# Performance work log

Hardware: AMD Instinct MI355X
Metric: run time of the kernel (lower is better)

The kernel has to match this reference:

```python
import jax, jax.numpy as jnp
import numpy as np

ALPHA = 0.2  # LeakyReLU negative slope


def setup_inputs() -> dict:
    key = jax.random.key(0)
    k1, k2, k3 = jax.random.split(key, 3)
    N, F_IN, F_OUT = 8192, 128, 64
    inputs = jax.random.normal(k1, (N, F_IN), dtype=jnp.float32)
    # xavier_uniform with gain=1.414
    limW = 1.414 * np.sqrt(6.0 / (F_IN + F_OUT))
    W = jax.random.uniform(k2, (F_IN, F_OUT), minval=-limW, maxval=limW, dtype=jnp.float32)
    lima = 1.414 * np.sqrt(6.0 / (2 * F_OUT + 1))
    a = jax.random.uniform(k3, (2 * F_OUT, 1), minval=-lima, maxval=lima, dtype=jnp.float32)
    return {"inputs": inputs, "W": W, "a": a}


def reference(inputs, W, a):
    F_OUT = W.shape[1]
    h = inputs @ W  # [N, F_out]
    # The torch code concatenates [h_i, h_j] and dots with a; equivalently
    # split a into a1 (for h_i) and a2 (for h_j): e_ij = LeakyReLU(h_i.a1 + h_j.a2)
    a1 = a[:F_OUT, 0]  # [F_out]
    a2 = a[F_OUT:, 0]  # [F_out]
    f1 = h @ a1  # [N]
    f2 = h @ a2  # [N]
    e = jax.nn.leaky_relu(f1[:, None] + f2[None, :], negative_slope=ALPHA)  # [N, N]
    attention = jax.nn.softmax(e, axis=1)  # dense GAT: softmax over all nodes
    # dropout=0.0 / eval mode -> identity
    feature = attention @ h  # [N, F_out]
    return jax.nn.elu(feature)  # concat=True branch
```

## Files before the change

kernel.cpp:

```cpp
#include <hip/hip_runtime.h>

#define NR    8192
#define ALPHA 0.2f
#define NCH   512
#define CSZ   16

__device__ inline unsigned enc_f32(float f) {
    unsigned u = __float_as_uint(f);
    return (u & 0x80000000u) ? ~u : (u | 0x80000000u);
}
__device__ inline float dec_f32(unsigned u) {
    return __uint_as_float((u & 0x80000000u) ? (u ^ 0x80000000u) : ~u);
}

__global__ __launch_bounds__(256) void kA(
    const float* __restrict__ X, const float* __restrict__ W, const float* __restrict__ aa,
    float* __restrict__ H, float* __restrict__ HT, float* __restrict__ F1,
    unsigned* __restrict__ ENC)
{
    __shared__ __align__(16) float xs[16 * 128];
    __shared__ float part[16 * 4 * 64];
    __shared__ float htl[64 * 17];
    const int tid = threadIdx.x, w = tid >> 6, c = tid & 63;
    const int R0 = blockIdx.x * 16;

    float Wreg[32];
#pragma unroll
    for (int e = 0; e < 32; ++e) Wreg[e] = W[(w * 32 + e) * 64 + c];
    {
        const float4* X4 = (const float4*)(X + R0 * 128);
        float4* xs4 = (float4*)xs;
        xs4[tid] = X4[tid];
        xs4[256 + tid] = X4[256 + tid];
    }
    __syncthreads();

    for (int r = 0; r < 16; ++r) {
        const float4* xr4 = (const float4*)&xs[r * 128 + w * 32];
        float acc = 0.f;
#pragma unroll
        for (int e = 0; e < 8; ++e) {
            float4 xv = xr4[e];
            acc = fmaf(xv.x, Wreg[e * 4 + 0], acc);
            acc = fmaf(xv.y, Wreg[e * 4 + 1], acc);
            acc = fmaf(xv.z, Wreg[e * 4 + 2], acc);
            acc = fmaf(xv.w, Wreg[e * 4 + 3], acc);
        }
        part[(r * 4 + w) * 64 + c] = acc;
    }
    __syncthreads();

    const float a1 = aa[c], a2 = aa[64 + c];
    for (int rr = 0; rr < 4; ++rr) {
        const int r = w * 4 + rr, i = R0 + r;
        float h = part[(r * 4 + 0) * 64 + c] + part[(r * 4 + 1) * 64 + c]
                + part[(r * 4 + 2) * 64 + c] + part[(r * 4 + 3) * 64 + c];
        H[i * 64 + c] = h;
        htl[c * 17 + r] = h;
        float v1 = h * a1, v2 = h * a2;
#pragma unroll
        for (int m = 32; m >= 1; m >>= 1) {
            v1 += __shfl_xor(v1, m, 64);
            v2 += __shfl_xor(v2, m, 64);
        }
        if (c == 0) { F1[i] = v1; ENC[i] = enc_f32(v2); }
    }
    __syncthreads();
    {
        const int ct = tid >> 2, rq = tid & 3;
        float4 v = make_float4(htl[ct * 17 + rq * 4 + 0], htl[ct * 17 + rq * 4 + 1],
                               htl[ct * 17 + rq * 4 + 2], htl[ct * 17 + rq * 4 + 3]);
        *(float4*)&HT[ct * NR + R0 + rq * 4] = v;
    }
}

__global__ __launch_bounds__(256) void kB(
    const unsigned* __restrict__ ENC, float* __restrict__ SF2, int* __restrict__ PERM)
{
    __shared__ unsigned cw[4 * 8];
    const int tid = threadIdx.x, bid = blockIdx.x;
    const uint4* E4 = (const uint4*)ENC;

    unsigned long long k64[32];
    {
        const unsigned base = tid * 4;
#pragma unroll
        for (int q = 0; q < 8; ++q) {
            uint4 v = E4[q * 256 + tid];
            const unsigned ib = q * 1024 + base;
            k64[q * 4 + 0] = ((unsigned long long)v.x << 13) | (ib + 0);
            k64[q * 4 + 1] = ((unsigned long long)v.y << 13) | (ib + 1);
            k64[q * 4 + 2] = ((unsigned long long)v.z << 13) | (ib + 2);
            k64[q * 4 + 3] = ((unsigned long long)v.w << 13) | (ib + 3);
        }
    }

    unsigned cnt[8];
#pragma unroll
    for (int jj = 0; jj < 8; ++jj) {
        const int j = bid * 8 + jj;
        const unsigned long long th = ((unsigned long long)ENC[j] << 13) | (unsigned)j;
        unsigned cjj = 0;
#pragma unroll
        for (int q = 0; q < 32; ++q) cjj += (unsigned)(k64[q] < th);
        cnt[jj] = cjj;
    }
#pragma unroll
    for (int jj = 0; jj < 8; ++jj) {
        unsigned v = cnt[jj];
#pragma unroll
        for (int m = 32; m >= 1; m >>= 1) v += (unsigned)__shfl_xor((int)v, m, 64);
        cnt[jj] = v;
    }
    const int w = tid >> 6;
    if ((tid & 63) == 0) {
#pragma unroll
        for (int jj = 0; jj < 8; ++jj) cw[w * 8 + jj] = cnt[jj];
    }
    __syncthreads();
    if (tid < 8) {
        const unsigned r = cw[tid] + cw[8 + tid] + cw[16 + tid] + cw[24 + tid];
        const int j = bid * 8 + tid;
        SF2[r] = dec_f32(ENC[j]);
        PERM[r] = j;
    }
}

__global__ __launch_bounds__(1024) void kC34(
    const float* __restrict__ HT, const float* __restrict__ SF2, const int* __restrict__ PERM,
    float4* __restrict__ SPQJ, float* __restrict__ CHPx, float* __restrict__ CHQx,
    float* __restrict__ cs)
{
    __shared__ float preP[1024], preQ[1024];
    __shared__ float scP[NCH], scQ[NCH];
    const int t = threadIdx.x, cb = blockIdx.x;
    const float fm = SF2[NR - 1];
    float accP = 0.f, accQ = 0.f;

    const float4* S4 = (const float4*)(SF2 + t * 8);
    const int4*   P4 = (const int4*)(PERM + t * 8);
    float4 f0 = S4[0], f1v = S4[1];
    int4   j0 = P4[0], j1 = P4[1];
    float sv[8] = { f0.x, f0.y, f0.z, f0.w, f1v.x, f1v.y, f1v.z, f1v.w };
    int   jx[8] = { j0.x, j0.y, j0.z, j0.w, j1.x, j1.y, j1.z, j1.w };

    if (cb < 64) {
        const float* __restrict__ hcol = HT + cb * NR;
#pragma unroll
        for (int e = 0; e < 8; ++e) {
            const float d = sv[e] - fm;
            const float P = __expf(d), Q = __expf(ALPHA * d);
            const float hv = hcol[jx[e]];
            accP = fmaf(P, hv, accP);
            accQ = fmaf(Q, hv, accQ);
        }
    } else {
#pragma unroll
        for (int e = 0; e < 8; ++e) {
            const float d = sv[e] - fm;
            const float P = __expf(d), Q = __expf(ALPHA * d);
            SPQJ[t * 8 + e] = make_float4(sv[e], P, Q, __int_as_float(jx[e]));
            accP += P; accQ += Q;
        }
        if (t < NCH) cs[t] = SF2[t * CSZ];
    }

    preP[t] = accP; preQ[t] = accQ;
    __syncthreads();
    if (t < NCH) {
        scP[t] = preP[2 * t] + preP[2 * t + 1];
        scQ[t] = preQ[2 * t] + preQ[2 * t + 1];
    }
    __syncthreads();
    for (int off = 1; off < NCH; off <<= 1) {
        float uP = 0.f, uQ = 0.f;
        if (t < NCH && t >= off) { uP = scP[t - off]; uQ = scQ[t - off]; }
        __syncthreads();
        if (t < NCH) { scP[t] += uP; scQ[t] += uQ; }
        __syncthreads();
    }
    if (t < NCH) {
        const float eP = (t > 0) ? scP[t - 1] : 0.f;
        const float eQ = (t > 0) ? scQ[t - 1] : 0.f;
        CHPx[t * 65 + cb] = eP;
        CHQx[t * 65 + cb] = eQ;
        if (t == NCH - 1) { CHPx[NCH * 65 + cb] = scP[t]; CHQx[NCH * 65 + cb] = scQ[t]; }
    }
}

__global__ __launch_bounds__(256) void kD(
    const float* __restrict__ H, const float* __restrict__ F1, const float* __restrict__ SF2,
    const float4* __restrict__ SPQJ, const float* __restrict__ CHPx,
    const float* __restrict__ CHQx, const float* __restrict__ cs, float* __restrict__ OUT)
{
    __shared__ float sb[NCH];
    const int tid = threadIdx.x, w = tid >> 6, c = tid & 63, bid = blockIdx.x;
    sb[tid] = cs[tid];
    sb[256 + tid] = cs[256 + tid];
    __syncthreads();

    const float fm = SF2[NR - 1];
    const float Ptot = CHPx[NCH * 65 + c], ptot = CHPx[NCH * 65 + 64];
    const int i = bid * 4 + w;

    const float f1 = F1[i];
    const float s = f1 + fm;
    const float mrow = fmaxf(s, ALPHA * s);
    const float A = __expf(s - mrow);
    const float B = __expf(ALPHA * s - mrow);
    const float th = -f1;

    int lo = 0, hi = NCH;
    while (lo < hi) { int mid = (lo + hi) >> 1; if (sb[mid] < th) lo = mid + 1; else hi = mid; }
    const int b = lo > 0 ? lo - 1 : 0;
    const int t0 = b * CSZ;

    float qv = CHQx[b * 65 + c],  pp = CHPx[b * 65 + c];
    float qs = CHQx[b * 65 + 64], ps = CHPx[b * 65 + 64];
#pragma unroll
    for (int tt = 0; tt < CSZ; ++tt) {
        const float4 v = SPQJ[t0 + tt];
        const int jv = __float_as_int(v.w);
        const float hv = H[jv * 64 + c];
        const bool cd = v.x < th;
        const float cP = cd ? v.y : 0.f, cQ = cd ? v.z : 0.f;
        qv = fmaf(cQ, hv, qv); qs += cQ;
        pp = fmaf(cP, hv, pp); ps += cP;
    }
    const float Pvec = Ptot - pp;
    const float pden = ptot - ps;
    const float num = A * Pvec + B * qv;
    const float den = A * pden + B * qs;
    const float feat = num / den;
    OUT[i * 64 + c] = feat > 0.f ? feat : expm1f(feat);
}

extern "C" void kernel_launch(void* const* d_in, const int* in_sizes, int n_in,
                              void* d_out, int out_size, void* d_ws, size_t ws_size,
                              hipStream_t stream) {
    const float* X = (const float*)d_in[0];
    const float* W = (const float*)d_in[1];
    const float* a = (const float*)d_in[2];
    float* OUT = (float*)d_out;

    float*    ws   = (float*)d_ws;
    float*    H    = ws;
    float*    HT   = H + 524288;
    float*    F1   = HT + 524288;
    unsigned* ENC  = (unsigned*)(F1 + 8192);
    float*    SF2  = (float*)(ENC + 8192);
    int*      PERM = (int*)(SF2 + 8192);
    float4*   SPQJ = (float4*)(PERM + 8192);
    float*    CHPx = (float*)(SPQJ + 8192);
    float*    CHQx = CHPx + 513 * 65;
    float*    cs   = CHQx + 513 * 65;

    kA  <<<512,  256,  0, stream>>>(X, W, a, H, HT, F1, ENC);
    kB  <<<1024, 256,  0, stream>>>(ENC, SF2, PERM);
    kC34<<<65,   1024, 0, stream>>>(HT, SF2, PERM, SPQJ, CHPx, CHQx, cs);
    kD  <<<2048, 256,  0, stream>>>(H, F1, SF2, SPQJ, CHPx, CHQx, cs, OUT);
}
```

Measured before the change: 39.07 us.

## Fuse prefix-scan and output kernels, compute exp weights in rank kernel

Removes the H row-major copy and the separate prefix-sum and output kernels. The rank kernel now computes the global max itself, along with the P/Q exponentials and chunk boundaries, and writes the sorted SPQJ array directly. A new fused kernel runs 256 blocks (64 columns × 4 row slices). Each block recomputes the column prefix scan in shared memory and then produces outputs for 2048 rows. This cuts one launch and the global round-trip of the chunk prefix arrays. The cost is that the scan is computed redundantly four times per column, and the output writes become strided by column.

```diff
diff --git a/kernel.cpp b/kernel.cpp
--- a/kernel.cpp
+++ b/kernel.cpp
@@ -15,8 +15,7 @@
 
 __global__ __launch_bounds__(256) void kA(
     const float* __restrict__ X, const float* __restrict__ W, const float* __restrict__ aa,
-    float* __restrict__ H, float* __restrict__ HT, float* __restrict__ F1,
-    unsigned* __restrict__ ENC)
+    float* __restrict__ HT, float* __restrict__ F1, unsigned* __restrict__ ENC)
 {
     __shared__ __align__(16) float xs[16 * 128];
     __shared__ float part[16 * 4 * 64];
@@ -55,7 +54,6 @@
         const int r = w * 4 + rr, i = R0 + r;
         float h = part[(r * 4 + 0) * 64 + c] + part[(r * 4 + 1) * 64 + c]
                 + part[(r * 4 + 2) * 64 + c] + part[(r * 4 + 3) * 64 + c];
-        H[i * 64 + c] = h;
         htl[c * 17 + r] = h;
         float v1 = h * a1, v2 = h * a2;
 #pragma unroll
@@ -75,18 +73,21 @@
 }
 
 __global__ __launch_bounds__(256) void kB(
-    const unsigned* __restrict__ ENC, float* __restrict__ SF2, int* __restrict__ PERM)
+    const unsigned* __restrict__ ENC, float4* __restrict__ SPQJ,
+    float* __restrict__ cs, float* __restrict__ FMf)
 {
-    __shared__ unsigned cw[4 * 8];
+    __shared__ unsigned cw[32];
     const int tid = threadIdx.x, bid = blockIdx.x;
     const uint4* E4 = (const uint4*)ENC;
 
     unsigned long long k64[32];
+    unsigned mx = 0;
     {
         const unsigned base = tid * 4;
 #pragma unroll
         for (int q = 0; q < 8; ++q) {
             uint4 v = E4[q * 256 + tid];
+            mx = max(max(mx, v.x), max(max(v.y, v.z), v.w));
             const unsigned ib = q * 1024 + base;
             k64[q * 4 + 0] = ((unsigned long long)v.x << 13) | (ib + 0);
             k64[q * 4 + 1] = ((unsigned long long)v.y << 13) | (ib + 1);
@@ -94,6 +95,13 @@
             k64[q * 4 + 3] = ((unsigned long long)v.w << 13) | (ib + 3);
         }
     }
+#pragma unroll
+    for (int m = 32; m >= 1; m >>= 1)
+        mx = max(mx, (unsigned)__shfl_xor((int)mx, m, 64));
+    if ((tid & 63) == 0) cw[tid >> 6] = mx;
+    __syncthreads();
+    const float fm = dec_f32(max(max(cw[0], cw[1]), max(cw[2], cw[3])));
+    __syncthreads();
 
     unsigned cnt[8];
 #pragma unroll
@@ -121,118 +129,92 @@
     if (tid < 8) {
         const unsigned r = cw[tid] + cw[8 + tid] + cw[16 + tid] + cw[24 + tid];
         const int j = bid * 8 + tid;
-        SF2[r] = dec_f32(ENC[j]);
-        PERM[r] = j;
-    }
-}
-
-__global__ __launch_bounds__(1024) void kC34(
-    const float* __restrict__ HT, const float* __restrict__ SF2, const int* __restrict__ PERM,
-    float4* __restrict__ SPQJ, float* __restrict__ CHPx, float* __restrict__ CHQx,
-    float* __restrict__ cs)
+        const float f = dec_f32(ENC[j]);
+        const float d = f - fm;
+        const float P = __expf(d), Q = __expf(ALPHA * d);
+        SPQJ[r] = make_float4(f, P, Q, __int_as_float(j));
+        if ((r & (CSZ - 1)) == 0) cs[r >> 4] = f;
+    }
+    if (bid == 0 && tid == 0) FMf[0] = fm;
+}
+
+__global__ __launch_bounds__(1024) void kCD(
+    const float* __restrict__ HT, const float* __restrict__ F1,
+    const float4* __restrict__ SPQJ, const float* __restrict__ cs,
+    const float* __restrict__ FMf, float* __restrict__ OUT)
 {
-    __shared__ float preP[1024], preQ[1024];
-    __shared__ float scP[NCH], scQ[NCH];
-    const int t = threadIdx.x, cb = blockIdx.x;
-    const float fm = SF2[NR - 1];
-    float accP = 0.f, accQ = 0.f;
-
-    const float4* S4 = (const float4*)(SF2 + t * 8);
-    const int4*   P4 = (const int4*)(PERM + t * 8);
-    float4 f0 = S4[0], f1v = S4[1];
-    int4   j0 = P4[0], j1 = P4[1];
-    float sv[8] = { f0.x, f0.y, f0.z, f0.w, f1v.x, f1v.y, f1v.z, f1v.w };
-    int   jx[8] = { j0.x, j0.y, j0.z, j0.w, j1.x, j1.y, j1.z, j1.w };
-
-    if (cb < 64) {
-        const float* __restrict__ hcol = HT + cb * NR;
-#pragma unroll
-        for (int e = 0; e < 8; ++e) {
-            const float d = sv[e] - fm;
-            const float P = __expf(d), Q = __expf(ALPHA * d);
-            const float hv = hcol[jx[e]];
-            accP = fmaf(P, hv, accP);
-            accQ = fmaf(Q, hv, accQ);
-        }
-    } else {
-#pragma unroll
-        for (int e = 0; e < 8; ++e) {
-            const float d = sv[e] - fm;
-            const float P = __expf(d), Q = __expf(ALPHA * d);
-            SPQJ[t * 8 + e] = make_float4(sv[e], P, Q, __int_as_float(jx[e]));
-            accP += P; accQ += Q;
-        }
-        if (t < NCH) cs[t] = SF2[t * CSZ];
-    }
-
-    preP[t] = accP; preQ[t] = accQ;
+    __shared__ float preP[1024], preQ[1024], preS[1024], preT[1024];
+    __shared__ float scP[NCH], scQ[NCH], ssp[NCH], ssq[NCH];
+    __shared__ float csb[NCH];
+    const int t = threadIdx.x;
+    const int col = blockIdx.x & 63, slice = blockIdx.x >> 6;
+    const float* __restrict__ hcol = HT + col * NR;
+    const float fm = FMf[0];
+
+    float accP = 0.f, accQ = 0.f, sp = 0.f, sq = 0.f;
+#pragma unroll
+    for (int e = 0; e < 8; ++e) {
+        const float4 v = SPQJ[t * 8 + e];
+        const float hv = hcol[__float_as_int(v.w)];
+        accP = fmaf(v.y, hv, accP);
+        accQ = fmaf(v.z, hv, accQ);
+        sp += v.y; sq += v.z;
+    }
+    preP[t] = accP; preQ[t] = accQ; preS[t] = sp; preT[t] = sq;
+    if (t < NCH) csb[t] = cs[t];
     __syncthreads();
     if (t < NCH) {
         scP[t] = preP[2 * t] + preP[2 * t + 1];
         scQ[t] = preQ[2 * t] + preQ[2 * t + 1];
+        ssp[t] = preS[2 * t] + preS[2 * t + 1];
+        ssq[t] = preT[2 * t] + preT[2 * t + 1];
     }
     __syncthreads();
     for (int off = 1; off < NCH; off <<= 1) {
-        float uP = 0.f, uQ = 0.f;
-        if (t < NCH && t >= off) { uP = scP[t - off]; uQ = scQ[t - off]; }
+        float uP = 0.f, uQ = 0.f, uS = 0.f, uT = 0.f;
+        if (t < NCH && t >= off) { uP = scP[t - off]; uQ = scQ[t - off];
+                                   uS = ssp[t - off]; uT = ssq[t - off]; }
         __syncthreads();
-        if (t < NCH) { scP[t] += uP; scQ[t] += uQ; }
+        if (t < NCH) { scP[t] += uP; scQ[t] += uQ; ssp[t] += uS; ssq[t] += uT; }
         __syncthreads();
     }
-    if (t < NCH) {
-        const float eP = (t > 0) ? scP[t - 1] : 0.f;
-        const float eQ = (t > 0) ? scQ[t - 1] : 0.f;
-        CHPx[t * 65 + cb] = eP;
-        CHQx[t * 65 + cb] = eQ;
-        if (t == NCH - 1) { CHPx[NCH * 65 + cb] = scP[t]; CHQx[NCH * 65 + cb] = scQ[t]; }
-    }
-}
-
-__global__ __launch_bounds__(256) void kD(
-    const float* __restrict__ H, const float* __restrict__ F1, const float* __restrict__ SF2,
-    const float4* __restrict__ SPQJ, const float* __restrict__ CHPx,
-    const float* __restrict__ CHQx, const float* __restrict__ cs, float* __restrict__ OUT)
-{
-    __shared__ float sb[NCH];
-    const int tid = threadIdx.x, w = tid >> 6, c = tid & 63, bid = blockIdx.x;
-    sb[tid] = cs[tid];
-    sb[256 + tid] = cs[256 + tid];
-    __syncthreads();
-
-    const float fm = SF2[NR - 1];
-    const float Ptot = CHPx[NCH * 65 + c], ptot = CHPx[NCH * 65 + 64];
-    const int i = bid * 4 + w;
-
-    const float f1 = F1[i];
-    const float s = f1 + fm;
-    const float mrow = fmaxf(s, ALPHA * s);
-    const float A = __expf(s - mrow);
-    const float B = __expf(ALPHA * s - mrow);
-    const float th = -f1;
-
-    int lo = 0, hi = NCH;
-    while (lo < hi) { int mid = (lo + hi) >> 1; if (sb[mid] < th) lo = mid + 1; else hi = mid; }
-    const int b = lo > 0 ? lo - 1 : 0;
-    const int t0 = b * CSZ;
-
-    float qv = CHQx[b * 65 + c],  pp = CHPx[b * 65 + c];
-    float qs = CHQx[b * 65 + 64], ps = CHPx[b * 65 + 64];
-#pragma unroll
-    for (int tt = 0; tt < CSZ; ++tt) {
-        const float4 v = SPQJ[t0 + tt];
-        const int jv = __float_as_int(v.w);
-        const float hv = H[jv * 64 + c];
-        const bool cd = v.x < th;
-        const float cP = cd ? v.y : 0.f, cQ = cd ? v.z : 0.f;
-        qv = fmaf(cQ, hv, qv); qs += cQ;
-        pp = fmaf(cP, hv, pp); ps += cP;
-    }
-    const float Pvec = Ptot - pp;
-    const float pden = ptot - ps;
-    const float num = A * Pvec + B * qv;
-    const float den = A * pden + B * qs;
-    const float feat = num / den;
-    OUT[i * 64 + c] = feat > 0.f ? feat : expm1f(feat);
+    const float Ptot = scP[NCH - 1], ptot = ssp[NCH - 1];
+
+#pragma unroll
+    for (int q = 0; q < 2; ++q) {
+        const int i = slice * 2048 + q * 1024 + t;
+        const float f1 = F1[i];
+        const float s = f1 + fm;
+        const float mrow = fmaxf(s, ALPHA * s);
+        const float A = __expf(s - mrow);
+        const float B = __expf(ALPHA * s - mrow);
+        const float th = -f1;
+
+        int lo = 0, hi = NCH;
+        while (lo < hi) { int mid = (lo + hi) >> 1; if (csb[mid] < th) lo = mid + 1; else hi = mid; }
+        const int b = lo > 0 ? lo - 1 : 0;
+
+        float pp = (b > 0) ? scP[b - 1] : 0.f;
+        float qv = (b > 0) ? scQ[b - 1] : 0.f;
+        float ps = (b > 0) ? ssp[b - 1] : 0.f;
+        float qs = (b > 0) ? ssq[b - 1] : 0.f;
+        const int t0 = b * CSZ;
+#pragma unroll
+        for (int e = 0; e < CSZ; ++e) {
+            const float4 v = SPQJ[t0 + e];
+            const float hv = hcol[__float_as_int(v.w)];
+            const bool cd = v.x < th;
+            const float cP = cd ? v.y : 0.f, cQ = cd ? v.z : 0.f;
+            pp = fmaf(cP, hv, pp); ps += cP;
+            qv = fmaf(cQ, hv, qv); qs += cQ;
+        }
+        const float Pvec = Ptot - pp;
+        const float pden = ptot - ps;
+        const float num = A * Pvec + B * qv;
+        const float den = A * pden + B * qs;
+        const float feat = num / den;
+        OUT[i * 64 + col] = feat > 0.f ? feat : expm1f(feat);
+    }
 }
 
 extern "C" void kernel_launch(void* const* d_in, const int* in_sizes, int n_in,
@@ -244,19 +226,14 @@
     float* OUT = (float*)d_out;
 
     float*    ws   = (float*)d_ws;
-    float*    H    = ws;
-    float*    HT   = H + 524288;
+    float*    HT   = ws;
     float*    F1   = HT + 524288;
     unsigned* ENC  = (unsigned*)(F1 + 8192);
-    float*    SF2  = (float*)(ENC + 8192);
-    int*      PERM = (int*)(SF2 + 8192);
-    float4*   SPQJ = (float4*)(PERM + 8192);
-    float*    CHPx = (float*)(SPQJ + 8192);
-    float*    CHQx = CHPx + 513 * 65;
-    float*    cs   = CHQx + 513 * 65;
-
-    kA  <<<512,  256,  0, stream>>>(X, W, a, H, HT, F1, ENC);
-    kB  <<<1024, 256,  0, stream>>>(ENC, SF2, PERM);
-    kC34<<<65,   1024, 0, stream>>>(HT, SF2, PERM, SPQJ, CHPx, CHQx, cs);
-    kD  <<<2048, 256,  0, stream>>>(H, F1, SF2, SPQJ, CHPx, CHQx, cs, OUT);
-}
+    float*    FMf  = (float*)(ENC + 8192);
+    float*    cs   = FMf + 16;
+    float4*   SPQJ = (float4*)(cs + 512);
+
+    kA <<<512,  256,  0, stream>>>(X, W, a, HT, F1, ENC);
+    kB <<<1024, 256,  0, stream>>>(ENC, SPQJ, cs, FMf);
+    kCD<<<256,  1024, 0, stream>>>(HT, F1, SPQJ, cs, FMf, OUT);
+}
```

Measured after the change: 60.57 us. 1.55x slower.
